# Performance work log

Measured on AMD Instinct MI355X. Metric: run time of the kernel, lower is better.

The kernel has to match this reference:

```python
import jax, jax.numpy as jnp
import numpy as np

NU, NI, E, D = 100000, 50000, 500000, 64
L = 3  # number of NGCF layers
SLOPE = 0.2
EPS = 1e-12


def setup_inputs() -> dict:
    key = jax.random.key(0)
    ks = jax.random.split(key, 12)
    scale = 1.0 / np.sqrt(D)  # roughly xavier-ish magnitude
    return {
        "feat_user": jax.random.normal(ks[0], (NU, D), jnp.float32) * scale,
        "feat_item": jax.random.normal(ks[1], (NI, D), jnp.float32) * scale,
        "W1": jax.random.normal(ks[2], (L, D, D), jnp.float32) * scale,
        "b1": jnp.zeros((L, D), jnp.float32),
        "W2": jax.random.normal(ks[3], (L, D, D), jnp.float32) * scale,
        "b2": jnp.zeros((L, D), jnp.float32),
        "u_idx": jax.random.randint(ks[4], (E,), 0, NU),
        "i_idx": jax.random.randint(ks[5], (E,), 0, NI),
        "users": jax.random.randint(ks[6], (8192,), 0, NU),
        "pos_items": jax.random.randint(ks[7], (8192,), 0, NI),
        "neg_items": jax.random.randint(ks[8], (8192,), 0, NI),
    }


def _l2norm(h):
    n = jnp.sqrt(jnp.sum(h * h, axis=1, keepdims=True))
    return h / jnp.maximum(n, EPS)


def reference(feat_user, feat_item, W1, b1, W2, b2, u_idx, i_idx, users, pos_items, neg_items):
    # symmetric edge norm 1/sqrt(deg_u * deg_i), same for both directions
    ones = jnp.ones((E,), jnp.float32)
    deg_u = jax.ops.segment_sum(ones, u_idx, num_segments=NU)
    deg_i = jax.ops.segment_sum(ones, i_idx, num_segments=NI)
    norm = (deg_u[u_idx] * deg_i[i_idx]) ** -0.5  # [E]
    norm = norm[:, None]

    hu, hi = feat_user, feat_item
    user_embeds, item_embeds = [hu], [hi]
    for l in range(L):
        w1, bb1, w2, bb2 = W1[l], b1[l], W2[l], b2[l]
        pu = hu @ w1 + bb1  # self-loop message W1(h) per user node
        pi = hi @ w1 + bb1
        eu = hu[u_idx]      # [E, D] gathered src features
        ei = hi[i_idx]
        pw = (eu * ei) @ w2 + bb2  # shared elementwise-product term
        m_u2i = norm * (pu[u_idx] + pw)  # user -> item messages
        m_i2u = norm * (pi[i_idx] + pw)  # item -> user messages
        hu = pu + jax.ops.segment_sum(m_i2u, u_idx, num_segments=NU)
        hi = pi + jax.ops.segment_sum(m_u2i, i_idx, num_segments=NI)
        hu = _l2norm(jax.nn.leaky_relu(hu, SLOPE))
        hi = _l2norm(jax.nn.leaky_relu(hi, SLOPE))
        user_embeds.append(hu)
        item_embeds.append(hi)

    user_embd = jnp.concatenate(user_embeds, axis=1)  # [NU, (L+1)*D]
    item_embd = jnp.concatenate(item_embeds, axis=1)
    return (user_embd[users], item_embd[pos_items], item_embd[neg_items])
```

## Files before the change

kernel.cpp:

```cpp
#include <hip/hip_runtime.h>

#define NU_N 100000
#define NI_N 50000
#define NN_N 150000
#define E_N  500000
#define NSEL 8192
#define GB   18750
#define OB   1536

typedef short s8v __attribute__((ext_vector_type(8)));
typedef short s4v __attribute__((ext_vector_type(4)));
typedef float f4v __attribute__((ext_vector_type(4)));

__device__ __forceinline__ float bf2f(unsigned short h) {
  union { unsigned u; float f; } v; v.u = ((unsigned)h) << 16; return v.f;
}
__device__ __forceinline__ unsigned short f2bf(float f) {
  union { float f; unsigned u; } v; v.f = f;
  unsigned u = v.u;
  u += 0x7FFFu + ((u >> 16) & 1u);
  return (unsigned short)(u >> 16);
}

__global__ void k_build(const int* __restrict__ u_idx, const int* __restrict__ i_idx,
                        int* __restrict__ cnt,
                        unsigned short* __restrict__ nbrU, int* __restrict__ nbrI) {
  int t = blockIdx.x * blockDim.x + threadIdx.x;
  if (t >= E_N / 4) return;
  int e = t * 4;
  int4 uu = *(const int4*)(u_idx + e);
  int4 ii = *(const int4*)(i_idx + e);
  int u[4] = {uu.x, uu.y, uu.z, uu.w};
  int it[4] = {ii.x, ii.y, ii.z, ii.w};
  int su[4], si[4];
#pragma unroll
  for (int k = 0; k < 4; k++) su[k] = atomicAdd(cnt + u[k], 1);
#pragma unroll
  for (int k = 0; k < 4; k++) si[k] = atomicAdd(cnt + NU_N + it[k], 1);
#pragma unroll
  for (int k = 0; k < 4; k++) {
    if (su[k] < 32) nbrU[(u[k] << 5) + su[k]] = (unsigned short)it[k];
    if (si[k] < 64) nbrI[(it[k] << 6) + si[k]] = u[k];
  }
}

__global__ void k_meta(const int* __restrict__ cnt, float* __restrict__ rdeg) {
  int g = blockIdx.x * blockDim.x + threadIdx.x;
  if (g >= NN_N) return;
  int d = cnt[g];
  rdeg[g] = d > 0 ? 1.0f / sqrtf((float)d) : 0.0f;
}

__global__ void k_cvt(const float* __restrict__ fu, const float* __restrict__ fi,
                      unsigned short* __restrict__ h) {
  int t = blockIdx.x * blockDim.x + threadIdx.x;
  if (t >= NN_N * 8) return;
  int i = t * 8;
  const float* src = i < NU_N * 64 ? (fu + i) : (fi + (i - NU_N * 64));
  float4 a = *(const float4*)(src);
  float4 b = *(const float4*)(src + 4);
  s8v o;
  o[0] = (short)f2bf(a.x); o[1] = (short)f2bf(a.y);
  o[2] = (short)f2bf(a.z); o[3] = (short)f2bf(a.w);
  o[4] = (short)f2bf(b.x); o[5] = (short)f2bf(b.y);
  o[6] = (short)f2bf(b.z); o[7] = (short)f2bf(b.w);
  *(s8v*)(h + i) = o;
}

__global__ void k_cvtW(const float* __restrict__ w1, const float* __restrict__ w2,
                       unsigned short* __restrict__ o1, unsigned short* __restrict__ o2) {
  int t = blockIdx.x * blockDim.x + threadIdx.x;
  if (t >= 3 * 8 * 64) return;
  int lane = t & 63;
  int fk = (t >> 6) & 7;
  int l = t >> 9;
  int n = fk >> 1, kh = fk & 1;
  int lm = lane & 15, lqq = lane >> 4;
  int dst = l * 4096 + (fk << 9) + (lane << 3);
  s8v v1, v2;
#pragma unroll
  for (int j = 0; j < 8; j++) {
    int src = l * 4096 + (32 * kh + 8 * lqq + j) * 64 + 16 * n + lm;
    v1[j] = (short)f2bf(w1[src]);
    v2[j] = (short)f2bf(w2[src]);
  }
  *(s8v*)(o1 + dst) = v1;
  *(s8v*)(o2 + dst) = v2;
}

__device__ __forceinline__ void out_body(int t, const float* __restrict__ fu,
                                         const float* __restrict__ fi,
                                         const unsigned short* __restrict__ h,
                                         const int* __restrict__ users,
                                         const int* __restrict__ pos,
                                         const int* __restrict__ neg,
                                         float* __restrict__ out, int l) {
  int j4 = (t & 15) * 4;
  int row = (t >> 4) & (NSEL - 1);
  int grp = t >> 17;
  int sr = grp == 0 ? users[row] : (grp == 1 ? pos[row] : neg[row]);
  float4 v;
  if (l == 0) {
    const float* f = grp == 0 ? fu : fi;
    v = *(const float4*)(f + (size_t)sr * 64 + j4);
  } else {
    const unsigned short* hh = h + (size_t)(grp == 0 ? sr : NU_N + sr) * 64 + j4;
    s4v x = *(const s4v*)hh;
    v.x = bf2f((unsigned short)x[0]); v.y = bf2f((unsigned short)x[1]);
    v.z = bf2f((unsigned short)x[2]); v.w = bf2f((unsigned short)x[3]);
  }
  *(float4*)(out + (size_t)grp * NSEL * 256 + (size_t)row * 256 + (size_t)l * 64 + j4) = v;
}

template <int CSUM>
__global__ void k_gather(const unsigned short* __restrict__ h,
                         const int* __restrict__ cnt,
                         const unsigned short* __restrict__ nbrU, const int* __restrict__ nbrI,
                         const float* __restrict__ rdeg,
                         unsigned short* __restrict__ s, float* __restrict__ csum,
                         const float* __restrict__ fu, const float* __restrict__ fi,
                         const int* __restrict__ users, const int* __restrict__ pos,
                         const int* __restrict__ neg, float* __restrict__ out, int lslice) {
  if (blockIdx.x >= GB) {
    int t = (blockIdx.x - GB) * 256 + threadIdx.x;
    out_body(t, fu, fi, h, users, pos, neg, out, lslice);
    return;
  }
  int wv = (blockIdx.x * blockDim.x + threadIdx.x) >> 6;
  int lane = threadIdx.x & 63;
  int half = lane >> 5;
  int lane32 = lane & 31;
  int q = lane32 >> 3;
  int m = lane & 7;
  int g = wv * 2 + half;
  int d = cnt[g];
  bool isU = g < NU_N;
  int dcap = isU ? 32 : 64;
  d = d < dcap ? d : dcap;
  int k0 = isU ? (g << 5) : ((g - NU_N) << 6);
  float acc[8] = {0.f, 0.f, 0.f, 0.f, 0.f, 0.f, 0.f, 0.f};
  float c = 0.f;
  for (int s0 = q; s0 < d; s0 += 16) {
    int s1 = s0 + 4, s2 = s0 + 8, s3 = s0 + 12;
    int n0 = isU ? (NU_N + (int)nbrU[k0 + s0]) : nbrI[k0 + s0];
    int n1 = s1 < d ? (isU ? (NU_N + (int)nbrU[k0 + s1]) : nbrI[k0 + s1]) : NN_N;
    int n2 = s2 < d ? (isU ? (NU_N + (int)nbrU[k0 + s2]) : nbrI[k0 + s2]) : NN_N;
    int n3 = s3 < d ? (isU ? (NU_N + (int)nbrU[k0 + s3]) : nbrI[k0 + s3]) : NN_N;
    float w0 = rdeg[n0], w1 = rdeg[n1], w2 = rdeg[n2], w3 = rdeg[n3];
    if (CSUM) c += (w0 + w1) + (w2 + w3);
    s8v v0 = *(const s8v*)(h + (size_t)n0 * 64 + m * 8);
    s8v v1 = *(const s8v*)(h + (size_t)n1 * 64 + m * 8);
    s8v v2 = *(const s8v*)(h + (size_t)n2 * 64 + m * 8);
    s8v v3 = *(const s8v*)(h + (size_t)n3 * 64 + m * 8);
#pragma unroll
    for (int j = 0; j < 8; j++)
      acc[j] += (w0 * bf2f((unsigned short)v0[j]) + w1 * bf2f((unsigned short)v1[j])) +
                (w2 * bf2f((unsigned short)v2[j]) + w3 * bf2f((unsigned short)v3[j]));
  }
#pragma unroll
  for (int off = 8; off <= 16; off <<= 1) {
#pragma unroll
    for (int j = 0; j < 8; j++) acc[j] += __shfl_xor(acc[j], off);
    if (CSUM) c += __shfl_xor(c, off);
  }
  float rw = rdeg[g];
  if (q == 0) {
    s8v ov;
#pragma unroll
    for (int j = 0; j < 8; j++) ov[j] = (short)f2bf(acc[j] * rw);
    *(s8v*)(s + (size_t)g * 64 + m * 8) = ov;
    if (CSUM && m == 0) csum[g] = c;
  }
}

__global__ void k_update(unsigned short* __restrict__ h,
                         const unsigned short* __restrict__ s,
                         const float* __restrict__ csum, const float* __restrict__ rdeg,
                         const unsigned short* __restrict__ w1s, const unsigned short* __restrict__ w2s,
                         const float* __restrict__ b1, const float* __restrict__ b2) {
  int lane = threadIdx.x & 63;
  int lm = lane & 15, lq = lane >> 4;
  int tile = (blockIdx.x * blockDim.x + threadIdx.x) >> 6;
  if (tile >= NN_N / 16) return;
  s8v f1[4][2], f2w[4][2];
#pragma unroll
  for (int n = 0; n < 4; n++)
#pragma unroll
    for (int kh = 0; kh < 2; kh++) {
      int off = (((n << 1) | kh) << 9) + (lane << 3);
      f1[n][kh]  = *(const s8v*)(w1s + off);
      f2w[n][kh] = *(const s8v*)(w2s + off);
    }
  int m0 = tile << 4;
  size_t rowo = (size_t)(m0 + lm) * 64;
  s8v h0 = *(const s8v*)(h + rowo + 8 * lq);
  s8v h1 = *(const s8v*)(h + rowo + 32 + 8 * lq);
  s8v s0 = *(const s8v*)(s + rowo + 8 * lq);
  s8v s1 = *(const s8v*)(s + rowo + 32 + 8 * lq);
  s8v a10, a11, a20, a21;
#pragma unroll
  for (int j = 0; j < 8; j++) {
    float hv0 = bf2f((unsigned short)h0[j]), sv0 = bf2f((unsigned short)s0[j]);
    float hv1 = bf2f((unsigned short)h1[j]), sv1 = bf2f((unsigned short)s1[j]);
    a10[j] = (short)f2bf(hv0 + sv0); a20[j] = (short)f2bf(hv0 * sv0);
    a11[j] = (short)f2bf(hv1 + sv1); a21[j] = (short)f2bf(hv1 * sv1);
  }
  f4v c[4];
#pragma unroll
  for (int n = 0; n < 4; n++) c[n] = (f4v){0.f, 0.f, 0.f, 0.f};
#pragma unroll
  for (int n = 0; n < 4; n++) {
    c[n] = __builtin_amdgcn_mfma_f32_16x16x32_bf16(a10, f1[n][0], c[n], 0, 0, 0);
    c[n] = __builtin_amdgcn_mfma_f32_16x16x32_bf16(a11, f1[n][1], c[n], 0, 0, 0);
    c[n] = __builtin_amdgcn_mfma_f32_16x16x32_bf16(a20, f2w[n][0], c[n], 0, 0, 0);
    c[n] = __builtin_amdgcn_mfma_f32_16x16x32_bf16(a21, f2w[n][1], c[n], 0, 0, 0);
  }
  float b1c[4], b2c[4];
#pragma unroll
  for (int n = 0; n < 4; n++) { b1c[n] = b1[16 * n + lm]; b2c[n] = b2[16 * n + lm]; }
  float cm[4];
#pragma unroll
  for (int r = 0; r < 4; r++) {
    int row = m0 + 4 * lq + r;
    cm[r] = csum[row] * rdeg[row];
  }
  float x[4][4], ss[4] = {0.f, 0.f, 0.f, 0.f};
#pragma unroll
  for (int n = 0; n < 4; n++)
#pragma unroll
    for (int r = 0; r < 4; r++) {
      float v = c[n][r] + b1c[n] + cm[r] * (b1c[n] + b2c[n]);
      v = v > 0.0f ? v : 0.2f * v;
      x[n][r] = v;
      ss[r] += v * v;
    }
#pragma unroll
  for (int r = 0; r < 4; r++) {
#pragma unroll
    for (int off = 1; off < 16; off <<= 1) ss[r] += __shfl_xor(ss[r], off);
    ss[r] = 1.0f / fmaxf(sqrtf(ss[r]), 1e-12f);
  }
#pragma unroll
  for (int n = 0; n < 4; n++)
#pragma unroll
    for (int r = 0; r < 4; r++) {
      size_t o = (size_t)(m0 + 4 * lq + r) * 64 + 16 * n + lm;
      h[o] = f2bf(x[n][r] * ss[r]);
    }
}

__global__ void k_out(const float* __restrict__ fu, const float* __restrict__ fi,
                      const unsigned short* __restrict__ h,
                      const int* __restrict__ users, const int* __restrict__ pos,
                      const int* __restrict__ neg, float* __restrict__ out, int l) {
  int t = blockIdx.x * blockDim.x + threadIdx.x;
  if (t >= 3 * NSEL * 16) return;
  out_body(t, fu, fi, h, users, pos, neg, out, l);
}

extern "C" void kernel_launch(void* const* d_in, const int* in_sizes, int n_in,
                              void* d_out, int out_size, void* d_ws, size_t ws_size,
                              hipStream_t stream) {
  (void)in_sizes; (void)n_in; (void)out_size; (void)ws_size;
  const float* fu = (const float*)d_in[0];
  const float* fi = (const float*)d_in[1];
  const float* W1 = (const float*)d_in[2];
  const float* b1 = (const float*)d_in[3];
  const float* W2 = (const float*)d_in[4];
  const float* b2 = (const float*)d_in[5];
  const int* u_idx = (const int*)d_in[6];
  const int* i_idx = (const int*)d_in[7];
  const int* users = (const int*)d_in[8];
  const int* pos   = (const int*)d_in[9];
  const int* neg   = (const int*)d_in[10];
  float* out = (float*)d_out;

  char* w = (char*)d_ws;
  auto alloc = [&](size_t bytes) { char* p = w; w += (bytes + 255) & ~(size_t)255; return p; };
  unsigned short* h  = (unsigned short*)alloc((size_t)(NN_N + 1) * 64 * 2);
  unsigned short* sb = (unsigned short*)alloc((size_t)NN_N * 64 * 2);
  int*   cnt  = (int*)alloc((size_t)NN_N * 4);
  float* csum = (float*)alloc((size_t)NN_N * 4);
  float* rdeg = (float*)alloc((size_t)(NN_N + 1) * 4);
  unsigned short* nbrU = (unsigned short*)alloc((size_t)NU_N * 32 * 2);
  int*   nbrI = (int*)alloc((size_t)NI_N * 64 * 4);
  unsigned short* w1s = (unsigned short*)alloc((size_t)3 * 4096 * 2);
  unsigned short* w2s = (unsigned short*)alloc((size_t)3 * 4096 * 2);

  hipMemsetAsync(cnt, 0, (size_t)NN_N * 4, stream);
  hipMemsetAsync(h + (size_t)NN_N * 64, 0, 128, stream);
  hipMemsetAsync(rdeg + NN_N, 0, 4, stream);
  k_build<<<(E_N / 4 + 255) / 256, 256, 0, stream>>>(u_idx, i_idx, cnt, nbrU, nbrI);
  k_meta<<<(NN_N + 255) / 256, 256, 0, stream>>>(cnt, rdeg);
  k_cvt<<<(NN_N * 8 + 255) / 256, 256, 0, stream>>>(fu, fi, h);
  k_cvtW<<<(3 * 8 * 64 + 255) / 256, 256, 0, stream>>>(W1, W2, w1s, w2s);

  for (int l = 0; l < 3; l++) {
    if (l == 0)
      k_gather<1><<<GB + OB, 256, 0, stream>>>(h, cnt, nbrU, nbrI, rdeg, sb, csum,
                                               fu, fi, users, pos, neg, out, 0);
    else
      k_gather<0><<<GB + OB, 256, 0, stream>>>(h, cnt, nbrU, nbrI, rdeg, sb, csum,
                                               fu, fi, users, pos, neg, out, l);
    k_update<<<((NN_N / 16) * 64 + 255) / 256, 256, 0, stream>>>(
        h, sb, csum, rdeg, w1s + (size_t)l * 4096, w2s + (size_t)l * 4096,
        b1 + (size_t)l * 64, b2 + (size_t)l * 64);
  }
  k_out<<<(3 * NSEL * 16 + 255) / 256, 256, 0, stream>>>(fu, fi, h, users, pos, neg, out, 3);
}
```

Baseline: 237.9 us.

## Assign one 8-lane group per node in gather and merge prep kernels

The gather kernel previously gave each node 32 lanes, split into 4 neighbour slices, and combined them with cross-lane shuffles. It now assigns one 8-lane group per node, so each wave covers 8 nodes and each group walks the whole neighbour list sequentially with no shuffle reduction. This removes the reduction and the lanes left idle on low-degree nodes, at the cost of a longer serial loop per node and less memory-level parallelism for high-degree item nodes. Separately, the feature conversion, degree normalisation and weight conversion kernels are merged into one launch to cut launch overhead.

```diff
diff --git a/kernel.cpp b/kernel.cpp
--- a/kernel.cpp
+++ b/kernel.cpp
@@ -5,8 +5,11 @@
 #define NN_N 150000
 #define E_N  500000
 #define NSEL 8192
-#define GB   18750
+#define GB2  4688
 #define OB   1536
+#define MB   586
+#define CB   4688
+#define WB   6
 
 typedef short s8v __attribute__((ext_vector_type(8)));
 typedef short s4v __attribute__((ext_vector_type(4)));
@@ -44,48 +47,51 @@
   }
 }
 
-__global__ void k_meta(const int* __restrict__ cnt, float* __restrict__ rdeg) {
-  int g = blockIdx.x * blockDim.x + threadIdx.x;
-  if (g >= NN_N) return;
-  int d = cnt[g];
-  rdeg[g] = d > 0 ? 1.0f / sqrtf((float)d) : 0.0f;
-}
-
-__global__ void k_cvt(const float* __restrict__ fu, const float* __restrict__ fi,
-                      unsigned short* __restrict__ h) {
-  int t = blockIdx.x * blockDim.x + threadIdx.x;
-  if (t >= NN_N * 8) return;
-  int i = t * 8;
-  const float* src = i < NU_N * 64 ? (fu + i) : (fi + (i - NU_N * 64));
-  float4 a = *(const float4*)(src);
-  float4 b = *(const float4*)(src + 4);
-  s8v o;
-  o[0] = (short)f2bf(a.x); o[1] = (short)f2bf(a.y);
-  o[2] = (short)f2bf(a.z); o[3] = (short)f2bf(a.w);
-  o[4] = (short)f2bf(b.x); o[5] = (short)f2bf(b.y);
-  o[6] = (short)f2bf(b.z); o[7] = (short)f2bf(b.w);
-  *(s8v*)(h + i) = o;
-}
-
-__global__ void k_cvtW(const float* __restrict__ w1, const float* __restrict__ w2,
+__global__ void k_prep(const int* __restrict__ cnt, float* __restrict__ rdeg,
+                       const float* __restrict__ fu, const float* __restrict__ fi,
+                       unsigned short* __restrict__ h,
+                       const float* __restrict__ w1, const float* __restrict__ w2,
                        unsigned short* __restrict__ o1, unsigned short* __restrict__ o2) {
-  int t = blockIdx.x * blockDim.x + threadIdx.x;
-  if (t >= 3 * 8 * 64) return;
-  int lane = t & 63;
-  int fk = (t >> 6) & 7;
-  int l = t >> 9;
-  int n = fk >> 1, kh = fk & 1;
-  int lm = lane & 15, lqq = lane >> 4;
-  int dst = l * 4096 + (fk << 9) + (lane << 3);
-  s8v v1, v2;
-#pragma unroll
-  for (int j = 0; j < 8; j++) {
-    int src = l * 4096 + (32 * kh + 8 * lqq + j) * 64 + 16 * n + lm;
-    v1[j] = (short)f2bf(w1[src]);
-    v2[j] = (short)f2bf(w2[src]);
-  }
-  *(s8v*)(o1 + dst) = v1;
-  *(s8v*)(o2 + dst) = v2;
+  int b = blockIdx.x;
+  if (b < CB) {
+    int t = b * 256 + threadIdx.x;
+    int i = t * 8;
+    const float* src = i < NU_N * 64 ? (fu + i) : (fi + (i - NU_N * 64));
+    float4 a = *(const float4*)(src);
+    float4 bb = *(const float4*)(src + 4);
+    s8v o;
+    o[0] = (short)f2bf(a.x);  o[1] = (short)f2bf(a.y);
+    o[2] = (short)f2bf(a.z);  o[3] = (short)f2bf(a.w);
+    o[4] = (short)f2bf(bb.x); o[5] = (short)f2bf(bb.y);
+    o[6] = (short)f2bf(bb.z); o[7] = (short)f2bf(bb.w);
+    *(s8v*)(h + i) = o;
+    return;
+  }
+  if (b < CB + MB) {
+    int g = (b - CB) * 256 + threadIdx.x;
+    if (g >= NN_N) return;
+    int d = cnt[g];
+    rdeg[g] = d > 0 ? 1.0f / sqrtf((float)d) : 0.0f;
+    return;
+  }
+  {
+    int t = (b - CB - MB) * 256 + threadIdx.x;
+    int lane = t & 63;
+    int fk = (t >> 6) & 7;
+    int l = t >> 9;
+    int n = fk >> 1, kh = fk & 1;
+    int lm = lane & 15, lqq = lane >> 4;
+    int dst = l * 4096 + (fk << 9) + (lane << 3);
+    s8v v1, v2;
+#pragma unroll
+    for (int j = 0; j < 8; j++) {
+      int src = l * 4096 + (32 * kh + 8 * lqq + j) * 64 + 16 * n + lm;
+      v1[j] = (short)f2bf(w1[src]);
+      v2[j] = (short)f2bf(w2[src]);
+    }
+    *(s8v*)(o1 + dst) = v1;
+    *(s8v*)(o2 + dst) = v2;
+  }
 }
 
 __device__ __forceinline__ void out_body(int t, const float* __restrict__ fu,
@@ -121,18 +127,17 @@
                          const float* __restrict__ fu, const float* __restrict__ fi,
                          const int* __restrict__ users, const int* __restrict__ pos,
                          const int* __restrict__ neg, float* __restrict__ out, int lslice) {
-  if (blockIdx.x >= GB) {
-    int t = (blockIdx.x - GB) * 256 + threadIdx.x;
+  if (blockIdx.x >= GB2) {
+    int t = (blockIdx.x - GB2) * 256 + threadIdx.x;
     out_body(t, fu, fi, h, users, pos, neg, out, lslice);
     return;
   }
-  int wv = (blockIdx.x * blockDim.x + threadIdx.x) >> 6;
+  int wq = (blockIdx.x * blockDim.x + threadIdx.x) >> 6;
   int lane = threadIdx.x & 63;
-  int half = lane >> 5;
-  int lane32 = lane & 31;
-  int q = lane32 >> 3;
+  int grp = lane >> 3;
   int m = lane & 7;
-  int g = wv * 2 + half;
+  int g = wq * 8 + grp;
+  if (g >= NN_N) return;
   int d = cnt[g];
   bool isU = g < NU_N;
   int dcap = isU ? 32 : 64;
@@ -140,12 +145,11 @@
   int k0 = isU ? (g << 5) : ((g - NU_N) << 6);
   float acc[8] = {0.f, 0.f, 0.f, 0.f, 0.f, 0.f, 0.f, 0.f};
   float c = 0.f;
-  for (int s0 = q; s0 < d; s0 += 16) {
-    int s1 = s0 + 4, s2 = s0 + 8, s3 = s0 + 12;
+  for (int s0 = 0; s0 < d; s0 += 4) {
     int n0 = isU ? (NU_N + (int)nbrU[k0 + s0]) : nbrI[k0 + s0];
-    int n1 = s1 < d ? (isU ? (NU_N + (int)nbrU[k0 + s1]) : nbrI[k0 + s1]) : NN_N;
-    int n2 = s2 < d ? (isU ? (NU_N + (int)nbrU[k0 + s2]) : nbrI[k0 + s2]) : NN_N;
-    int n3 = s3 < d ? (isU ? (NU_N + (int)nbrU[k0 + s3]) : nbrI[k0 + s3]) : NN_N;
+    int n1 = s0 + 1 < d ? (isU ? (NU_N + (int)nbrU[k0 + s0 + 1]) : nbrI[k0 + s0 + 1]) : NN_N;
+    int n2 = s0 + 2 < d ? (isU ? (NU_N + (int)nbrU[k0 + s0 + 2]) : nbrI[k0 + s0 + 2]) : NN_N;
+    int n3 = s0 + 3 < d ? (isU ? (NU_N + (int)nbrU[k0 + s0 + 3]) : nbrI[k0 + s0 + 3]) : NN_N;
     float w0 = rdeg[n0], w1 = rdeg[n1], w2 = rdeg[n2], w3 = rdeg[n3];
     if (CSUM) c += (w0 + w1) + (w2 + w3);
     s8v v0 = *(const s8v*)(h + (size_t)n0 * 64 + m * 8);
@@ -157,20 +161,12 @@
       acc[j] += (w0 * bf2f((unsigned short)v0[j]) + w1 * bf2f((unsigned short)v1[j])) +
                 (w2 * bf2f((unsigned short)v2[j]) + w3 * bf2f((unsigned short)v3[j]));
   }
-#pragma unroll
-  for (int off = 8; off <= 16; off <<= 1) {
-#pragma unroll
-    for (int j = 0; j < 8; j++) acc[j] += __shfl_xor(acc[j], off);
-    if (CSUM) c += __shfl_xor(c, off);
-  }
   float rw = rdeg[g];
-  if (q == 0) {
-    s8v ov;
-#pragma unroll
-    for (int j = 0; j < 8; j++) ov[j] = (short)f2bf(acc[j] * rw);
-    *(s8v*)(s + (size_t)g * 64 + m * 8) = ov;
-    if (CSUM && m == 0) csum[g] = c;
-  }
+  s8v ov;
+#pragma unroll
+  for (int j = 0; j < 8; j++) ov[j] = (short)f2bf(acc[j] * rw);
+  *(s8v*)(s + (size_t)g * 64 + m * 8) = ov;
+  if (CSUM && m == 0) csum[g] = c;
 }
 
 __global__ void k_update(unsigned short* __restrict__ h,
@@ -291,17 +287,15 @@
   hipMemsetAsync(h + (size_t)NN_N * 64, 0, 128, stream);
   hipMemsetAsync(rdeg + NN_N, 0, 4, stream);
   k_build<<<(E_N / 4 + 255) / 256, 256, 0, stream>>>(u_idx, i_idx, cnt, nbrU, nbrI);
-  k_meta<<<(NN_N + 255) / 256, 256, 0, stream>>>(cnt, rdeg);
-  k_cvt<<<(NN_N * 8 + 255) / 256, 256, 0, stream>>>(fu, fi, h);
-  k_cvtW<<<(3 * 8 * 64 + 255) / 256, 256, 0, stream>>>(W1, W2, w1s, w2s);
+  k_prep<<<CB + MB + WB, 256, 0, stream>>>(cnt, rdeg, fu, fi, h, W1, W2, w1s, w2s);
 
   for (int l = 0; l < 3; l++) {
     if (l == 0)
-      k_gather<1><<<GB + OB, 256, 0, stream>>>(h, cnt, nbrU, nbrI, rdeg, sb, csum,
-                                               fu, fi, users, pos, neg, out, 0);
+      k_gather<1><<<GB2 + OB, 256, 0, stream>>>(h, cnt, nbrU, nbrI, rdeg, sb, csum,
+                                                fu, fi, users, pos, neg, out, 0);
     else
-      k_gather<0><<<GB + OB, 256, 0, stream>>>(h, cnt, nbrU, nbrI, rdeg, sb, csum,
-                                               fu, fi, users, pos, neg, out, l);
+      k_gather<0><<<GB2 + OB, 256, 0, stream>>>(h, cnt, nbrU, nbrI, rdeg, sb, csum,
+                                                fu, fi, users, pos, neg, out, l);
     k_update<<<((NN_N / 16) * 64 + 255) / 256, 256, 0, stream>>>(
         h, sb, csum, rdeg, w1s + (size_t)l * 4096, w2s + (size_t)l * 4096,
         b1 + (size_t)l * 64, b2 + (size_t)l * 64);
```

After: 214.1 us. 1.11x faster.
